# Optimization experiments

Hardware: AMD Instinct MI355X
Metric: run time of the kernel (lower is better)

Reference implementation:

```python
import jax, jax.numpy as jnp
import numpy as np

N_QUBITS = 4
N_LAYERS = 2


def _apply_1q(state, gate, wire):
    # state: [B,2,2,2,2] complex; gate: [2,2] or [B,2,2] complex
    ax = wire + 1
    st = jnp.moveaxis(state, ax, 1)  # [B,2,...]
    if gate.ndim == 2:
        st = jnp.einsum('ij,bj...->bi...', gate, st)
    else:
        st = jnp.einsum('bij,bj...->bi...', gate, st)
    return jnp.moveaxis(st, 1, ax)


def _cnot(state, control, target):
    ca, ta = control + 1, target + 1
    s0 = jnp.take(state, 0, axis=ca)
    s1 = jnp.take(state, 1, axis=ca)
    ta2 = ta - 1 if ta > ca else ta  # axis shift after take
    s1 = jnp.flip(s1, axis=ta2)      # flip target when control=1
    return jnp.stack([s0, s1], axis=ca)


def _rx(theta):  # theta: [B] -> [B,2,2]
    c = jnp.cos(theta / 2).astype(jnp.complex64)
    s = jnp.sin(theta / 2).astype(jnp.complex64)
    return jnp.stack([jnp.stack([c, -1j * s], -1),
                      jnp.stack([-1j * s, c], -1)], -2)


def _ry(theta):  # scalar -> [2,2]
    c = jnp.cos(theta / 2).astype(jnp.complex64)
    s = jnp.sin(theta / 2).astype(jnp.complex64)
    return jnp.stack([jnp.stack([c, -s]), jnp.stack([s, c])])


def _rz(theta):  # scalar -> [2,2] diag(e^{-i t/2}, e^{i t/2})
    half = (theta / 2).astype(jnp.complex64)
    z = jnp.zeros((), jnp.complex64)
    return jnp.stack([jnp.stack([jnp.exp(-1j * half), z]),
                      jnp.stack([z, jnp.exp(1j * half)])])


def _circuit(angles, wq):
    # angles: [B,4] float32; wq: [2,4,3] float32 -> [B,4] expval PauliZ
    B = angles.shape[0]
    state = jnp.zeros((B, 2, 2, 2, 2), jnp.complex64)
    state = state.at[:, 0, 0, 0, 0].set(1.0)
    for i in range(N_QUBITS):
        state = _apply_1q(state, _rx(angles[:, i]), i)
    for layer in range(N_LAYERS):
        for i in range(N_QUBITS):
            state = _apply_1q(state, _rz(wq[layer, i, 0]), i)
            state = _apply_1q(state, _ry(wq[layer, i, 1]), i)
            state = _apply_1q(state, _rz(wq[layer, i, 2]), i)
        for i in range(N_QUBITS - 1):
            state = _cnot(state, i, i + 1)
    probs = state.real ** 2 + state.imag ** 2  # [B,2,2,2,2]
    zs = []
    for i in range(N_QUBITS):
        axes = tuple(a for a in range(1, 5) if a != i + 1)
        marg = jnp.sum(probs, axis=axes)  # [B,2]
        zs.append(marg[:, 0] - marg[:, 1])
    return jnp.stack(zs, axis=-1)  # [B,4]


def setup_inputs() -> dict:
    key = jax.random.key(0)
    ks = jax.random.split(key, 8)
    B, F = 262144, 64
    x = jax.random.normal(ks[0], (B, F), jnp.float32)
    Wp = jax.random.normal(ks[1], (N_QUBITS, F), jnp.float32) * (1.0 / np.sqrt(F))
    bp = jnp.zeros((N_QUBITS,), jnp.float32)
    wq = 0.01 * jax.random.normal(ks[2], (N_LAYERS, N_QUBITS, 3), jnp.float32)
    W1 = jax.random.normal(ks[3], (64, N_QUBITS), jnp.float32) * 0.5
    b1 = jnp.zeros((64,), jnp.float32)
    W2 = jax.random.normal(ks[4], (1, 64), jnp.float32) * 0.125
    b2 = jnp.zeros((1,), jnp.float32)
    return {"x": x, "Wp": Wp, "bp": bp, "wq": wq, "W1": W1, "b1": b1, "W2": W2, "b2": b2}


def reference(x, Wp, bp, wq, W1, b1, W2, b2):
    angles = x @ Wp.T + bp               # feature_projector -> [B,4]
    q_out = _circuit(angles, wq)         # [B,4]
    h = jax.nn.relu(q_out @ W1.T + b1)   # [B,64]
    return h @ W2.T + b2                 # [B,1]
```

## Files before the change

kernel.cpp:

```cpp
#include <hip/hip_runtime.h>
#include <hip/hip_bf16.h>

#define CBUF_N 1157


__device__ inline void gate_rz(float* ar, float* ai, int q, float th) {
    float c = cosf(0.5f * th), s = sinf(0.5f * th);
    int st = 8 >> q;
    #pragma unroll
    for (int k = 0; k < 16; k++) {
        float r = ar[k], im = ai[k];
        if (k & st) {
            ar[k] = r * c - im * s;
            ai[k] = im * c + r * s;
        } else {
            ar[k] = r * c + im * s;
            ai[k] = im * c - r * s;
        }
    }
}

__device__ inline void gate_ry(float* ar, float* ai, int q, float th) {
    float c = cosf(0.5f * th), s = sinf(0.5f * th);
    int st = 8 >> q;
    #pragma unroll
    for (int k = 0; k < 16; k++) {
        if (!(k & st)) {
            int k1 = k | st;
            float r0 = ar[k], i0 = ai[k], r1 = ar[k1], i1 = ai[k1];
            ar[k]  = c * r0 - s * r1;  ai[k]  = c * i0 - s * i1;
            ar[k1] = s * r0 + c * r1;  ai[k1] = s * i0 + c * i1;
        }
    }
}

__device__ inline void gate_cnot(float* ar, float* ai, int c, int t) {
    int stc = 8 >> c, stt = 8 >> t;
    #pragma unroll
    for (int k = 0; k < 16; k++) {
        if ((k & stc) && !(k & stt)) {
            int k1 = k | stt;
            float r = ar[k], im = ai[k];
            ar[k] = ar[k1]; ai[k] = ai[k1];
            ar[k1] = r;     ai[k1] = im;
        }
    }
}

__global__ void precompute_kernel(const float* __restrict__ Wp,
                                  const float* __restrict__ bp,
                                  const float* __restrict__ wq,
                                  const float* __restrict__ W1,
                                  const float* __restrict__ b1,
                                  const float* __restrict__ W2,
                                  const float* __restrict__ b2,
                                  float* __restrict__ ws) {
    int t = threadIdx.x;

    if (t < 16) {
        float ar[16], ai[16];
        #pragma unroll
        for (int k = 0; k < 16; k++) { ar[k] = 0.f; ai[k] = 0.f; }
        ar[t] = 1.f;

        for (int layer = 0; layer < 2; layer++) {
            for (int q = 0; q < 4; q++) {
                const float* w = &wq[(layer * 4 + q) * 3];
                gate_rz(ar, ai, q, w[0]);
                gate_ry(ar, ai, q, w[1]);
                gate_rz(ar, ai, q, w[2]);
            }
            for (int c = 0; c < 3; c++) gate_cnot(ar, ai, c, c + 1);
        }

        int pc = __popc(t) & 3;
        #pragma unroll
        for (int j = 0; j < 16; j++) {
            float re = ar[j], im = ai[j], vr, vi;
            switch (pc) {
                case 0: vr = re;  vi = im;  break;
                case 1: vr = im;  vi = -re; break;
                case 2: vr = -re; vi = -im; break;
                case 3: vr = -im; vi = re;  break;
            }
            ws[j * 16 + t]       = vr;
            ws[256 + j * 16 + t] = vi;
        }
    }

    for (int q = 0; q < 4; q++) ws[512 + t * 4 + q] = Wp[q * 64 + t];
    if (t < 4) ws[768 + t] = bp[t];

    ws[772 + t * 6 + 0] = W1[t * 4 + 0];
    ws[772 + t * 6 + 1] = W1[t * 4 + 1];
    ws[772 + t * 6 + 2] = W1[t * 4 + 2];
    ws[772 + t * 6 + 3] = W1[t * 4 + 3];
    ws[772 + t * 6 + 4] = b1[t];
    ws[772 + t * 6 + 5] = W2[t];
    if (t == 0) ws[1156] = b2[0];
}


__global__ __launch_bounds__(256) void qmain_kernel(const float* __restrict__ x,
                                                    const float* __restrict__ cb,
                                                    float* __restrict__ out,
                                                    int B) {
    __shared__ float tile[256 * 33];
    const int t = threadIdx.x;
    const long row0 = (long)blockIdx.x * 256;
    const float* xb = x + row0 * 64;

    float ang[4];
    #pragma unroll
    for (int q = 0; q < 4; q++) ang[q] = cb[768 + q];

    #pragma unroll
    for (int s = 0; s < 2; s++) {
        if (s) __syncthreads();
        #pragma unroll
        for (int r = 0; r < 8; r++) {
            int idx = r * 1024 + t * 4;
            int row = idx >> 5;
            int col = idx & 31;
            float4 v = *reinterpret_cast<const float4*>(xb + row * 64 + s * 32 + col);
            float* dst = &tile[row * 33 + col];
            dst[0] = v.x; dst[1] = v.y; dst[2] = v.z; dst[3] = v.w;
        }
        __syncthreads();
        const float* myrow = &tile[t * 33];
        #pragma unroll
        for (int i = 0; i < 32; i++) {
            float xv = myrow[i];
            const float* w = &cb[512 + (s * 32 + i) * 4];
            #pragma unroll
            for (int q = 0; q < 4; q++) ang[q] = fmaf(xv, w[q], ang[q]);
        }
    }

    float c[4], s4[4];
    #pragma unroll
    for (int q = 0; q < 4; q++) {
        __sincosf(0.5f * ang[q], &s4[q], &c[q]);
    }
    float pre[4]  = { c[0] * c[1], c[0] * s4[1], s4[0] * c[1], s4[0] * s4[1] };
    float post[4] = { c[2] * c[3], c[2] * s4[3], s4[2] * c[3], s4[2] * s4[3] };
    float m[16];
    #pragma unroll
    for (int k = 0; k < 16; k++) m[k] = pre[k >> 2] * post[k & 3];

    float z0 = 0.f, z1 = 0.f, z2 = 0.f, z3 = 0.f;
    #pragma unroll
    for (int j = 0; j < 16; j++) {
        const float* vr = &cb[j * 16];
        const float* vi = &cb[256 + j * 16];
        float re = 0.f, im = 0.f;
        #pragma unroll
        for (int k = 0; k < 16; k++) {
            re = fmaf(vr[k], m[k], re);
            im = fmaf(vi[k], m[k], im);
        }
        float p = re * re + im * im;
        z0 += (j & 8) ? -p : p;
        z1 += (j & 4) ? -p : p;
        z2 += (j & 2) ? -p : p;
        z3 += (j & 1) ? -p : p;
    }

    float acc = cb[1156];
    #pragma unroll
    for (int j = 0; j < 64; j++) {
        const float* mp = &cb[772 + j * 6];
        float h = mp[4];
        h = fmaf(mp[0], z0, h);
        h = fmaf(mp[1], z1, h);
        h = fmaf(mp[2], z2, h);
        h = fmaf(mp[3], z3, h);
        h = fmaxf(h, 0.f);
        acc = fmaf(mp[5], h, acc);
    }
    out[row0 + t] = acc;
}


extern "C" void kernel_launch(void* const* d_in, const int* in_sizes, int n_in,
                              void* d_out, int out_size, void* d_ws, size_t ws_size,
                              hipStream_t stream) {
    const float* x  = (const float*)d_in[0];
    const float* Wp = (const float*)d_in[1];
    const float* bp = (const float*)d_in[2];
    const float* wq = (const float*)d_in[3];
    const float* W1 = (const float*)d_in[4];
    const float* b1 = (const float*)d_in[5];
    const float* W2 = (const float*)d_in[6];
    const float* b2 = (const float*)d_in[7];
    float* ws = (float*)d_ws;
    float* out = (float*)d_out;

    int B = in_sizes[0] / 64;

    precompute_kernel<<<1, 64, 0, stream>>>(Wp, bp, wq, W1, b1, W2, b2, ws);

    int grid = (B + 255) / 256;
    qmain_kernel<<<grid, 256, 0, stream>>>(x, ws, out, B);
}
```

Baseline: 124.6 us.

## Prefetch all x loads into registers and use float4 LDS stores/loads

Both halves of the block's x tile are now issued as global float4 loads into registers up front, so the second half's latency overlaps the first half's compute. The shared tile is padded to a 36-float stride so rows can be written and read with float4 LDS operations instead of scalar ones. Launch bounds now request 4 blocks per CU. The cost is 64 extra registers per thread for the prefetched data, which may push register pressure against the occupancy target and risk spills.

```diff
diff --git a/kernel.cpp b/kernel.cpp
--- a/kernel.cpp
+++ b/kernel.cpp
@@ -101,39 +101,77 @@
 }
 
 
-__global__ __launch_bounds__(256) void qmain_kernel(const float* __restrict__ x,
-                                                    const float* __restrict__ cb,
-                                                    float* __restrict__ out,
-                                                    int B) {
-    __shared__ float tile[256 * 33];
+__global__ __launch_bounds__(256, 4) void qmain_kernel(const float* __restrict__ x,
+                                                       const float* __restrict__ cb,
+                                                       float* __restrict__ out,
+                                                       int B) {
+    __shared__ float tile[256 * 36];
     const int t = threadIdx.x;
     const long row0 = (long)blockIdx.x * 256;
     const float* xb = x + row0 * 64;
 
+    const int lrow = t >> 3;
+    const int lcol = (t & 7) * 4;
+
+    float4 v0[8];
+    #pragma unroll
+    for (int r = 0; r < 8; r++) {
+        int row = r * 32 + lrow;
+        v0[r] = *reinterpret_cast<const float4*>(xb + row * 64 + lcol);
+    }
+    float4 v1[8];
+    #pragma unroll
+    for (int r = 0; r < 8; r++) {
+        int row = r * 32 + lrow;
+        v1[r] = *reinterpret_cast<const float4*>(xb + row * 64 + 32 + lcol);
+    }
+
     float ang[4];
     #pragma unroll
     for (int q = 0; q < 4; q++) ang[q] = cb[768 + q];
 
     #pragma unroll
-    for (int s = 0; s < 2; s++) {
-        if (s) __syncthreads();
-        #pragma unroll
-        for (int r = 0; r < 8; r++) {
-            int idx = r * 1024 + t * 4;
-            int row = idx >> 5;
-            int col = idx & 31;
-            float4 v = *reinterpret_cast<const float4*>(xb + row * 64 + s * 32 + col);
-            float* dst = &tile[row * 33 + col];
-            dst[0] = v.x; dst[1] = v.y; dst[2] = v.z; dst[3] = v.w;
-        }
-        __syncthreads();
-        const float* myrow = &tile[t * 33];
-        #pragma unroll
-        for (int i = 0; i < 32; i++) {
-            float xv = myrow[i];
-            const float* w = &cb[512 + (s * 32 + i) * 4];
+    for (int r = 0; r < 8; r++) {
+        int row = r * 32 + lrow;
+        *reinterpret_cast<float4*>(&tile[row * 36 + lcol]) = v0[r];
+    }
+    __syncthreads();
+    {
+        const float4* myrow4 = reinterpret_cast<const float4*>(&tile[t * 36]);
+        #pragma unroll
+        for (int i = 0; i < 8; i++) {
+            float4 xv = myrow4[i];
+            const float* w = &cb[512 + (i * 4) * 4];
             #pragma unroll
-            for (int q = 0; q < 4; q++) ang[q] = fmaf(xv, w[q], ang[q]);
+            for (int q = 0; q < 4; q++) {
+                ang[q] = fmaf(xv.x, w[q],      ang[q]);
+                ang[q] = fmaf(xv.y, w[4 + q],  ang[q]);
+                ang[q] = fmaf(xv.z, w[8 + q],  ang[q]);
+                ang[q] = fmaf(xv.w, w[12 + q], ang[q]);
+            }
+        }
+    }
+    __syncthreads();
+
+    #pragma unroll
+    for (int r = 0; r < 8; r++) {
+        int row = r * 32 + lrow;
+        *reinterpret_cast<float4*>(&tile[row * 36 + lcol]) = v1[r];
+    }
+    __syncthreads();
+    {
+        const float4* myrow4 = reinterpret_cast<const float4*>(&tile[t * 36]);
+        #pragma unroll
+        for (int i = 0; i < 8; i++) {
+            float4 xv = myrow4[i];
+            const float* w = &cb[512 + (32 + i * 4) * 4];
+            #pragma unroll
+            for (int q = 0; q < 4; q++) {
+                ang[q] = fmaf(xv.x, w[q],      ang[q]);
+                ang[q] = fmaf(xv.y, w[4 + q],  ang[q]);
+                ang[q] = fmaf(xv.z, w[8 + q],  ang[q]);
+                ang[q] = fmaf(xv.w, w[12 + q], ang[q]);
+            }
         }
     }
 
```

Measured after the change: 136.7 us. 9.7% more time.

## Replace LDS-tiled projection with register-direct quad-split dot products and DPP reduction

Applied to the files above, without the earlier changes.

Drops the shared-memory transpose tile for the feature projection. Each lane now loads 16 contiguous floats of a row directly into registers, double-buffered across four rounds. Four lanes share a row and combine their partial dot products with DPP quad reductions; the result is kept by the lane whose sub-index matches the round, and output order is restored with ds_bpermute. This removes LDS traffic and barriers at the cost of more registers (the 64 projection weights are held per lane) and a launch-bounds occupancy hint. The grid now assumes B is a multiple of 256.

```diff
diff --git a/kernel.cpp b/kernel.cpp
--- a/kernel.cpp
+++ b/kernel.cpp
@@ -101,41 +101,70 @@
 }
 
 
-__global__ __launch_bounds__(256) void qmain_kernel(const float* __restrict__ x,
-                                                    const float* __restrict__ cb,
-                                                    float* __restrict__ out,
-                                                    int B) {
-    __shared__ float tile[256 * 33];
-    const int t = threadIdx.x;
-    const long row0 = (long)blockIdx.x * 256;
-    const float* xb = x + row0 * 64;
-
-    float ang[4];
-    #pragma unroll
-    for (int q = 0; q < 4; q++) ang[q] = cb[768 + q];
-
-    #pragma unroll
-    for (int s = 0; s < 2; s++) {
-        if (s) __syncthreads();
-        #pragma unroll
-        for (int r = 0; r < 8; r++) {
-            int idx = r * 1024 + t * 4;
-            int row = idx >> 5;
-            int col = idx & 31;
-            float4 v = *reinterpret_cast<const float4*>(xb + row * 64 + s * 32 + col);
-            float* dst = &tile[row * 33 + col];
-            dst[0] = v.x; dst[1] = v.y; dst[2] = v.z; dst[3] = v.w;
-        }
-        __syncthreads();
-        const float* myrow = &tile[t * 33];
-        #pragma unroll
-        for (int i = 0; i < 32; i++) {
-            float xv = myrow[i];
-            const float* w = &cb[512 + (s * 32 + i) * 4];
+__device__ __forceinline__ float quad_allsum(float v) {
+    v += __int_as_float(__builtin_amdgcn_mov_dpp(__float_as_int(v), 0xB1, 0xF, 0xF, true));
+    v += __int_as_float(__builtin_amdgcn_mov_dpp(__float_as_int(v), 0x4E, 0xF, 0xF, true));
+    return v;
+}
+
+__global__ __launch_bounds__(256, 3) void qmain_kernel(const float* __restrict__ x,
+                                                       const float* __restrict__ cb,
+                                                       float* __restrict__ out,
+                                                       int B) {
+    const int lane = threadIdx.x & 63;
+    const int wv   = threadIdx.x >> 6;
+    const long rows_base = (long)blockIdx.x * 256 + wv * 64;
+    const float* xw = x + rows_base * 64;
+    const int sub = lane & 3;
+
+    const float4* cb4 = reinterpret_cast<const float4*>(cb);
+    float4 wreg[16];
+    #pragma unroll
+    for (int j = 0; j < 16; j++) wreg[j] = cb4[128 + sub * 16 + j];
+
+    float ang0 = cb[768], ang1 = cb[769], ang2 = cb[770], ang3 = cb[771];
+
+    float4 cur[4], nxt[4];
+    {
+        const float* p = xw + lane * 16;
+        #pragma unroll
+        for (int j = 0; j < 4; j++) cur[j] = *reinterpret_cast<const float4*>(p + 4 * j);
+    }
+
+    #pragma unroll
+    for (int r = 0; r < 4; r++) {
+        if (r < 3) {
+            const float* p = xw + (r + 1) * 1024 + lane * 16;
             #pragma unroll
-            for (int q = 0; q < 4; q++) ang[q] = fmaf(xv, w[q], ang[q]);
-        }
-    }
+            for (int j = 0; j < 4; j++) nxt[j] = *reinterpret_cast<const float4*>(p + 4 * j);
+        }
+        float p0 = 0.f, p1 = 0.f, p2 = 0.f, p3 = 0.f;
+        #pragma unroll
+        for (int j = 0; j < 4; j++) {
+            float4 xv = cur[j];
+            float4 w0 = wreg[j * 4 + 0];
+            float4 w1 = wreg[j * 4 + 1];
+            float4 w2 = wreg[j * 4 + 2];
+            float4 w3 = wreg[j * 4 + 3];
+            p0 = fmaf(xv.x, w0.x, p0); p1 = fmaf(xv.x, w0.y, p1);
+            p2 = fmaf(xv.x, w0.z, p2); p3 = fmaf(xv.x, w0.w, p3);
+            p0 = fmaf(xv.y, w1.x, p0); p1 = fmaf(xv.y, w1.y, p1);
+            p2 = fmaf(xv.y, w1.z, p2); p3 = fmaf(xv.y, w1.w, p3);
+            p0 = fmaf(xv.z, w2.x, p0); p1 = fmaf(xv.z, w2.y, p1);
+            p2 = fmaf(xv.z, w2.z, p2); p3 = fmaf(xv.z, w2.w, p3);
+            p0 = fmaf(xv.w, w3.x, p0); p1 = fmaf(xv.w, w3.y, p1);
+            p2 = fmaf(xv.w, w3.z, p2); p3 = fmaf(xv.w, w3.w, p3);
+        }
+        float r0 = quad_allsum(p0);
+        float r1 = quad_allsum(p1);
+        float r2 = quad_allsum(p2);
+        float r3 = quad_allsum(p3);
+        if (sub == r) { ang0 += r0; ang1 += r1; ang2 += r2; ang3 += r3; }
+        #pragma unroll
+        for (int j = 0; j < 4; j++) cur[j] = nxt[j];
+    }
+
+    float ang[4] = { ang0, ang1, ang2, ang3 };
 
     float c[4], s4[4];
     #pragma unroll
@@ -178,7 +207,10 @@
         h = fmaxf(h, 0.f);
         acc = fmaf(mp[5], h, acc);
     }
-    out[row0 + t] = acc;
+
+    int srcb = (((lane & 15) * 4) + (lane >> 4)) * 4;
+    float accL = __int_as_float(__builtin_amdgcn_ds_bpermute(srcb, __float_as_int(acc)));
+    out[rows_base + lane] = accL;
 }
 
 
@@ -200,6 +232,6 @@
 
     precompute_kernel<<<1, 64, 0, stream>>>(Wp, bp, wq, W1, b1, W2, b2, ws);
 
-    int grid = (B + 255) / 256;
+    int grid = B / 256;
     qmain_kernel<<<grid, 256, 0, stream>>>(x, ws, out, B);
 }
```

New measurement: 131.5 us. +5.6%, slower.
